# Kernel optimization log

Hardware: AMD Instinct MI355X
Metric: run time of the kernel (lower is better)

The kernel has to match this reference:

```python
import jax, jax.numpy as jnp
import numpy as np

B, T, D, H = 16, 2048, 1024, 1024  # batch, seq (effective block_size), n_embed, head_size


def setup_inputs() -> dict:
    key = jax.random.key(0)
    k1, k2, k3, k4 = jax.random.split(key, 4)
    x = jax.random.normal(k1, (B, T, D), dtype=jnp.float32)
    # torch Linear weight is [out,in]; store as [in,out] for x @ W
    s = 1.0 / np.sqrt(D)
    Wq = jax.random.uniform(k2, (D, H), dtype=jnp.float32, minval=-s, maxval=s)
    Wk = jax.random.uniform(k3, (D, H), dtype=jnp.float32, minval=-s, maxval=s)
    Wv = jax.random.uniform(k4, (D, H), dtype=jnp.float32, minval=-s, maxval=s)
    return {"x": x, "Wq": Wq, "Wk": Wk, "Wv": Wv}


def reference(x, Wq, Wk, Wv):
    # Single-head causal self-attention, NO 1/sqrt(d) scaling (faithful to source).
    q = x @ Wq  # [B,T,H]
    k = x @ Wk  # [B,T,H]
    v = x @ Wv  # [B,T,H]
    w = jnp.einsum('bth,bsh->bts', q, k)  # [B,T,T]
    Tn = x.shape[1]
    causal = jnp.tril(jnp.ones((Tn, Tn), dtype=bool))
    w = jnp.where(causal, w, -jnp.inf)
    w = jax.nn.softmax(w, axis=-1)
    # dropout is identity in eval mode
    out = jnp.einsum('bts,bsh->bth', w, v)  # [B,T,H]
    return out
```

## Files before the change

### kernel.cpp

```cpp
#include <hip/hip_runtime.h>
#include <hip/hip_bf16.h>


typedef _Float16 half8 __attribute__((ext_vector_type(8)));
typedef _Float16 half4v __attribute__((ext_vector_type(4)));
typedef float floatx4 __attribute__((ext_vector_type(4)));

#define TB 16
#define TT 2048
#define TD 1024

#define BARRIER() asm volatile("s_barrier" ::: "memory")

__global__ void cvt_f32_f16(const float* __restrict__ in, _Float16* __restrict__ out, long n) {
    long i = ((long)blockIdx.x * blockDim.x + threadIdx.x) * 4;
    long stride = (long)gridDim.x * blockDim.x * 4;
    for (; i < n; i += stride) {
        float4 f = *(const float4*)(in + i);
        half4v h;
        h[0] = (_Float16)f.x; h[1] = (_Float16)f.y;
        h[2] = (_Float16)f.z; h[3] = (_Float16)f.w;
        *(half4v*)(out + i) = h;
    }
}

__global__ void transpose_cvt_w(const float* __restrict__ in, _Float16* __restrict__ out) {
    __shared__ float tile[32][33];
    const int bx = blockIdx.x * 32, by = blockIdx.y * 32;
    const int tx = threadIdx.x, ty = threadIdx.y;
#pragma unroll
    for (int i = ty; i < 32; i += 8) tile[i][tx] = in[(long)(by + i) * 1024 + bx + tx];
    __syncthreads();
#pragma unroll
    for (int i = ty; i < 32; i += 8) out[(long)(bx + i) * 1024 + by + tx] = (_Float16)tile[tx][i];
}

__device__ __forceinline__ void gload16(const _Float16* g, _Float16* l) {
    __builtin_amdgcn_global_load_lds((const __attribute__((address_space(1))) void*)g,
                                     (__attribute__((address_space(3))) void*)l, 16, 0, 0);
}

template <int MODE>
__global__ __launch_bounds__(512, 2) void gemm256(const _Float16* __restrict__ A,
                                                  const _Float16* __restrict__ B,
                                                  void* __restrict__ Cout,
                                                  void* __restrict__ Cout2,
                                                  int K, int lda, int ldb, int ldc,
                                                  long sAb, long sBb, long sCb,
                                                  int tilesN, int tilesM, int nb) {
    __shared__ _Float16 lds[65536];
    const int tid = threadIdx.x, lane = tid & 63, w = tid >> 6;
    const int wr = w >> 2, wc = w & 3;

    int b, ti, tj;
    if (MODE == 2) {
        const int grp = nb * 4;
        const int g = blockIdx.x / grp;
        ti = tilesM - 1 - g;
        int i2 = blockIdx.x - g * grp;
        const int q = grp >> 3, r = grp & 7, xcd = i2 & 7, idx = i2 >> 3;
        i2 = (xcd < r ? xcd * (q + 1) : r * (q + 1) + (xcd - r) * q) + idx;
        b = i2 >> 2; tj = i2 & 3;
    } else {
        int bx = blockIdx.x;
        const int nwg = gridDim.x, q = nwg >> 3, r = nwg & 7, xcd = bx & 7, idx = bx >> 3;
        bx = (xcd < r ? xcd * (q + 1) : r * (q + 1) + (xcd - r) * q) + idx;
        b = blockIdx.y;
        if (MODE == 1) {
            int rd = bx; ti = 0;
            while (rd > ti) { rd -= ti + 1; ++ti; }
            tj = rd;
        } else {
            ti = bx / tilesN; tj = bx % tilesN;
        }
    }
    A += (long)b * sAb;
    B += (long)b * sBb;
    const long m0 = (long)ti * 256, n0 = (long)tj * 256;
    const int nkt = (MODE == 2) ? (ti + 1) * 4 : (K >> 6);

    const int row0 = tid >> 2;
    const int co   = (((tid & 3) ^ ((tid >> 3) & 3)) << 3);
    const int fcol = ((((lane >> 4) ^ (lane >> 1)) & 3) << 3);
    const int arow = wr * 128 + (lane & 15);
    const int brow = wc * 64 + (lane & 15);

    auto Abase = [&](int buf, int kk) { return lds + ((buf * 2 + kk) << 13); };
    auto Bbase = [&](int buf, int kk) { return lds + 32768 + ((buf * 2 + kk) << 13); };

    auto stageA = [&](int buf, int kk, int kt) {
        const long kb = (long)kt * 64 + kk * 32 + co;
        _Float16* d = Abase(buf, kk) + (w << 9);
        gload16(A + (m0 + row0) * (long)lda + kb, d);
        gload16(A + (m0 + row0 + 128) * (long)lda + kb, d + 4096);
    };
    auto stageB = [&](int buf, int kk, int kt) {
        const long kb = (long)kt * 64 + kk * 32 + co;
        _Float16* d = Bbase(buf, kk) + (w << 9);
        gload16(B + (n0 + row0) * (long)ldb + kb, d);
        gload16(B + (n0 + row0 + 128) * (long)ldb + kb, d + 4096);
    };
    auto ldA = [&](int buf, int kk, int m) {
        return *(const half8*)(Abase(buf, kk) + (arow + m * 16) * 32 + fcol);
    };
    auto ldB = [&](int buf, int kk, int n) {
        return *(const half8*)(Bbase(buf, kk) + (brow + n * 16) * 32 + fcol);
    };

    floatx4 acc[8][4] = {};
    half8 afE[4], afO[4], bfE[4], bfO[4];

#define MFMA_Q(MH, BF, AF)                                                             \
    __builtin_amdgcn_s_setprio(1);                                                     \
    _Pragma("unroll") for (int mm = 0; mm < 4; ++mm)                                   \
    _Pragma("unroll") for (int nn = 0; nn < 4; ++nn)                                   \
        acc[(MH)*4 + mm][nn] =                                                         \
            __builtin_amdgcn_mfma_f32_16x16x32_f16(AF[mm], BF[nn], acc[(MH)*4 + mm][nn], 0, 0, 0); \
    __builtin_amdgcn_s_setprio(0);

    {
        const int k1 = (1 < nkt) ? 1 : nkt - 1;
        stageA(0, 0, 0); stageB(0, 0, 0);
        stageA(0, 1, 0); stageB(0, 1, 0);
        stageA(1, 0, k1); stageB(1, 0, k1);
    }
    asm volatile("s_waitcnt vmcnt(8)" ::: "memory");
    BARRIER();
#pragma unroll
    for (int nn = 0; nn < 4; ++nn) bfE[nn] = ldB(0, 0, nn);
#pragma unroll
    for (int mm = 0; mm < 4; ++mm) afE[mm] = ldA(0, 0, mm);

    for (int t = 0; t < nkt; ++t) {
        const int cur = t & 1, nxt = cur ^ 1;
        const int kt1 = (t + 1 < nkt) ? t + 1 : nkt - 1;
        const int kt2 = (t + 2 < nkt) ? t + 2 : nkt - 1;
        MFMA_Q(0, bfE, afE)
#pragma unroll
        for (int mm = 0; mm < 4; ++mm) afO[mm] = ldA(cur, 0, mm + 4);
        stageA(nxt, 1, kt1);
        asm volatile("s_waitcnt vmcnt(6)" ::: "memory");
        BARRIER();
        MFMA_Q(1, bfE, afO)
#pragma unroll
        for (int nn = 0; nn < 4; ++nn) bfO[nn] = ldB(cur, 1, nn);
#pragma unroll
        for (int mm = 0; mm < 4; ++mm) afE[mm] = ldA(cur, 1, mm);
        stageB(nxt, 1, kt1);
        BARRIER();
        MFMA_Q(0, bfO, afE)
#pragma unroll
        for (int mm = 0; mm < 4; ++mm) afO[mm] = ldA(cur, 1, mm + 4);
        stageA(cur, 0, kt2);
        asm volatile("s_waitcnt vmcnt(6)" ::: "memory");
        BARRIER();
        MFMA_Q(1, bfO, afO)
#pragma unroll
        for (int nn = 0; nn < 4; ++nn) bfE[nn] = ldB(nxt, 0, nn);
#pragma unroll
        for (int mm = 0; mm < 4; ++mm) afE[mm] = ldA(nxt, 0, mm);
        stageB(cur, 0, kt2);
        BARRIER();
    }
#undef MFMA_Q
    asm volatile("s_waitcnt vmcnt(0) lgkmcnt(0)" ::: "memory");

    const int r4 = (lane >> 4) * 4, ccol = lane & 15;
    if (MODE != 2) {
        _Float16* C;
        long nb0 = n0;
        if (MODE == 3 && n0 >= TD) { C = (_Float16*)Cout2; nb0 = n0 - TD; }
        else                        C = (_Float16*)Cout + (long)b * sCb;
#pragma unroll
        for (int m = 0; m < 8; ++m) {
            const long rbase = m0 + wr * 128 + m * 16 + r4;
#pragma unroll
            for (int n = 0; n < 4; ++n) {
                const long cbase = nb0 + wc * 64 + n * 16 + ccol;
#pragma unroll
                for (int j = 0; j < 4; ++j)
                    C[(rbase + j) * (long)ldc + cbase] = (_Float16)acc[m][n][j];
            }
        }
    } else {
        float* C = (float*)Cout + (long)b * sCb;
#pragma unroll
        for (int m = 0; m < 8; ++m) {
            const long rbase = m0 + wr * 128 + m * 16 + r4;
#pragma unroll
            for (int n = 0; n < 4; ++n) {
                const long cbase = n0 + wc * 64 + n * 16 + ccol;
#pragma unroll
                for (int j = 0; j < 4; ++j)
                    C[(rbase + j) * (long)ldc + cbase] = acc[m][n][j];
            }
        }
    }
}

__global__ __launch_bounds__(256) void softmax_rows_f16(_Float16* __restrict__ S, int T) {
    const int wv = threadIdx.x >> 6, lane = threadIdx.x & 63;
    const long row = (long)blockIdx.x * 4 + wv;
    const int t = (int)(row & (T - 1));
    _Float16* s = S + row * (long)T;
    const int nstore = ((t >> 8) + 1) << 8;

    float v[4][8];
    float mx = -__builtin_inff();
#pragma unroll
    for (int c = 0; c < 4; ++c) {
        const int col0 = (c * 64 + lane) * 8;
        if (col0 <= t) {
            half8 hv = *(const half8*)(s + col0);
#pragma unroll
            for (int j = 0; j < 8; ++j) {
                v[c][j] = (col0 + j <= t) ? (float)hv[j] : -__builtin_inff();
                mx = fmaxf(mx, v[c][j]);
            }
        } else {
#pragma unroll
            for (int j = 0; j < 8; ++j) v[c][j] = -__builtin_inff();
        }
    }
#pragma unroll
    for (int o = 32; o; o >>= 1) mx = fmaxf(mx, __shfl_xor(mx, o));

    float sum = 0.f;
#pragma unroll
    for (int c = 0; c < 4; ++c)
#pragma unroll
        for (int j = 0; j < 8; ++j) {
            float p = __expf(v[c][j] - mx);
            v[c][j] = p;
            sum += p;
        }
#pragma unroll
    for (int o = 32; o; o >>= 1) sum += __shfl_xor(sum, o);
    const float inv = 1.f / sum;

#pragma unroll
    for (int c = 0; c < 4; ++c) {
        const int col0 = (c * 64 + lane) * 8;
        if (col0 < nstore) {
            half8 o;
#pragma unroll
            for (int j = 0; j < 8; ++j) o[j] = (_Float16)(v[c][j] * inv);
            *(half8*)(s + col0) = o;
        }
    }
}

extern "C" void kernel_launch(void* const* d_in, const int* in_sizes, int n_in,
                              void* d_out, int out_size, void* d_ws, size_t ws_size,
                              hipStream_t stream) {
    const float* x  = (const float*)d_in[0];
    const float* Wq = (const float*)d_in[1];
    const float* Wk = (const float*)d_in[2];
    const float* Wv = (const float*)d_in[3];
    float* out = (float*)d_out;

    const size_t XB = (size_t)TB * TT * TD;

    _Float16* x16 = (_Float16*)d_out;
    _Float16* Kh  = (_Float16*)d_out + XB;

    char* ws = (char*)d_ws;
    size_t off = 0;
    auto carve = [&](size_t bytes) { char* p = ws + off; off = (off + bytes + 255) & ~(size_t)255; return p; };
    _Float16* wqt = (_Float16*)carve((size_t)TD * TD * 2);
    _Float16* wkt = (_Float16*)carve((size_t)TD * TD * 2);
    _Float16* wvt = (_Float16*)carve((size_t)TD * TD * 2);
    _Float16* Qh  = (_Float16*)carve(XB * 2);
    _Float16* Vt  = (_Float16*)carve(XB * 2);

    const size_t CH = (size_t)TT * TT * 2;
    int NB = 16;
    while (NB > 1 && off + (size_t)NB * CH > ws_size) NB >>= 1;
    _Float16* Sc = (_Float16*)carve((size_t)NB * CH);

    cvt_f32_f16<<<2048, 256, 0, stream>>>(x, x16, (long)XB);
    transpose_cvt_w<<<dim3(32, 32), dim3(32, 8), 0, stream>>>(Wq, wqt);
    transpose_cvt_w<<<dim3(32, 32), dim3(32, 8), 0, stream>>>(Wk, wkt);
    transpose_cvt_w<<<dim3(32, 32), dim3(32, 8), 0, stream>>>(Wv, wvt);

    gemm256<3><<<dim3(128 * 8, 1), 512, 0, stream>>>(x16, wqt, Qh, Kh, TD, TD, TD, TD,
                                                     0, 0, 0, 8, 128, 0);
    gemm256<0><<<dim3(4 * 8, TB), 512, 0, stream>>>(wvt, x16, Vt, nullptr, TD, TD, TD, TT,
                                                    0, (long)TT * TD, (long)TD * TT, 8, 4, 0);

    for (int cb = 0; cb < TB; cb += NB) {
        gemm256<1><<<dim3(36, NB), 512, 0, stream>>>(Qh + (size_t)cb * TT * TD,
                                                     Kh + (size_t)cb * TT * TD, Sc, nullptr,
                                                     TD, TD, TD, TT,
                                                     (long)TT * TD, (long)TT * TD, (long)TT * TT, 8, 8, 0);
        softmax_rows_f16<<<NB * TT / 4, 256, 0, stream>>>(Sc, TT);
        gemm256<2><<<dim3(NB * 32, 1), 512, 0, stream>>>(Sc, Vt + (size_t)cb * TD * TT,
                                                         out + (size_t)cb * TT * TD, nullptr, TT,
                                                         TT, TT, TD,
                                                         (long)TT * TT, (long)TD * TT, (long)TT * TD, 4, 8, NB);
    }
}
```

Before: 473.2 us.

## Switch GEMM inner product to 32x32x16 MFMA tiles with matching fragment layout

Replaces the 16x16x32 f16 MFMA with the 32x32x16 variant. This changes the accumulator shape to 4x2 floatx16 per wave, remaps the LDS fragment loads (row and column swizzle) and rewrites the epilogue's output row mapping. The larger MFMA tile means fewer instructions and fewer LDS operand reads per FLOP. The main loop is also unrolled by 2. The risk is mistakes in the lane-to-element mapping and higher register pressure.

Measured after the change: 497.1 us. 1.05x slower.

```diff
diff --git a/kernel.cpp b/kernel.cpp
--- a/kernel.cpp
+++ b/kernel.cpp
@@ -4,7 +4,7 @@
 
 typedef _Float16 half8 __attribute__((ext_vector_type(8)));
 typedef _Float16 half4v __attribute__((ext_vector_type(4)));
-typedef float floatx4 __attribute__((ext_vector_type(4)));
+typedef float floatx16 __attribute__((ext_vector_type(16)));
 
 #define TB 16
 #define TT 2048
@@ -81,9 +81,9 @@
 
     const int row0 = tid >> 2;
     const int co   = (((tid & 3) ^ ((tid >> 3) & 3)) << 3);
-    const int fcol = ((((lane >> 4) ^ (lane >> 1)) & 3) << 3);
-    const int arow = wr * 128 + (lane & 15);
-    const int brow = wc * 64 + (lane & 15);
+    const int rxor = (lane >> 1) & 3;
+    const int arowb = wr * 128 + (lane & 31);
+    const int browb = wc * 64 + (lane & 31);
 
     auto Abase = [&](int buf, int kk) { return lds + ((buf * 2 + kk) << 13); };
     auto Bbase = [&](int buf, int kk) { return lds + 32768 + ((buf * 2 + kk) << 13); };
@@ -100,22 +100,25 @@
         gload16(B + (n0 + row0) * (long)ldb + kb, d);
         gload16(B + (n0 + row0 + 128) * (long)ldb + kb, d + 4096);
     };
-    auto ldA = [&](int buf, int kk, int m) {
-        return *(const half8*)(Abase(buf, kk) + (arow + m * 16) * 32 + fcol);
+    auto ldA = [&](int buf, int kk, int mt, int kq) {
+        const int fcol = ((((kq << 1) | (lane >> 5)) ^ rxor) << 3);
+        return *(const half8*)(Abase(buf, kk) + (arowb + mt * 32) * 32 + fcol);
     };
-    auto ldB = [&](int buf, int kk, int n) {
-        return *(const half8*)(Bbase(buf, kk) + (brow + n * 16) * 32 + fcol);
+    auto ldB = [&](int buf, int kk, int nt, int kq) {
+        const int fcol = ((((kq << 1) | (lane >> 5)) ^ rxor) << 3);
+        return *(const half8*)(Bbase(buf, kk) + (browb + nt * 32) * 32 + fcol);
     };
 
-    floatx4 acc[8][4] = {};
+    floatx16 acc[4][2] = {};
     half8 afE[4], afO[4], bfE[4], bfO[4];
 
 #define MFMA_Q(MH, BF, AF)                                                             \
     __builtin_amdgcn_s_setprio(1);                                                     \
-    _Pragma("unroll") for (int mm = 0; mm < 4; ++mm)                                   \
-    _Pragma("unroll") for (int nn = 0; nn < 4; ++nn)                                   \
-        acc[(MH)*4 + mm][nn] =                                                         \
-            __builtin_amdgcn_mfma_f32_16x16x32_f16(AF[mm], BF[nn], acc[(MH)*4 + mm][nn], 0, 0, 0); \
+    _Pragma("unroll") for (int kq = 0; kq < 2; ++kq)                                   \
+    _Pragma("unroll") for (int ml = 0; ml < 2; ++ml)                                   \
+    _Pragma("unroll") for (int nt = 0; nt < 2; ++nt)                                   \
+        acc[(MH)*2 + ml][nt] = __builtin_amdgcn_mfma_f32_32x32x16_f16(                 \
+            AF[ml * 2 + kq], BF[nt * 2 + kq], acc[(MH)*2 + ml][nt], 0, 0, 0);          \
     __builtin_amdgcn_s_setprio(0);
 
     {
@@ -127,72 +130,75 @@
     asm volatile("s_waitcnt vmcnt(8)" ::: "memory");
     BARRIER();
 #pragma unroll
-    for (int nn = 0; nn < 4; ++nn) bfE[nn] = ldB(0, 0, nn);
-#pragma unroll
-    for (int mm = 0; mm < 4; ++mm) afE[mm] = ldA(0, 0, mm);
-
+    for (int i = 0; i < 4; ++i) bfE[i] = ldB(0, 0, i >> 1, i & 1);
+#pragma unroll
+    for (int i = 0; i < 4; ++i) afE[i] = ldA(0, 0, i >> 1, i & 1);
+
+#pragma unroll 2
     for (int t = 0; t < nkt; ++t) {
         const int cur = t & 1, nxt = cur ^ 1;
         const int kt1 = (t + 1 < nkt) ? t + 1 : nkt - 1;
         const int kt2 = (t + 2 < nkt) ? t + 2 : nkt - 1;
         MFMA_Q(0, bfE, afE)
 #pragma unroll
-        for (int mm = 0; mm < 4; ++mm) afO[mm] = ldA(cur, 0, mm + 4);
+        for (int i = 0; i < 4; ++i) afO[i] = ldA(cur, 0, 2 + (i >> 1), i & 1);
         stageA(nxt, 1, kt1);
         asm volatile("s_waitcnt vmcnt(6)" ::: "memory");
         BARRIER();
         MFMA_Q(1, bfE, afO)
 #pragma unroll
-        for (int nn = 0; nn < 4; ++nn) bfO[nn] = ldB(cur, 1, nn);
-#pragma unroll
-        for (int mm = 0; mm < 4; ++mm) afE[mm] = ldA(cur, 1, mm);
+        for (int i = 0; i < 4; ++i) bfO[i] = ldB(cur, 1, i >> 1, i & 1);
+#pragma unroll
+        for (int i = 0; i < 4; ++i) afE[i] = ldA(cur, 1, i >> 1, i & 1);
         stageB(nxt, 1, kt1);
         BARRIER();
         MFMA_Q(0, bfO, afE)
 #pragma unroll
-        for (int mm = 0; mm < 4; ++mm) afO[mm] = ldA(cur, 1, mm + 4);
+        for (int i = 0; i < 4; ++i) afO[i] = ldA(cur, 1, 2 + (i >> 1), i & 1);
         stageA(cur, 0, kt2);
         asm volatile("s_waitcnt vmcnt(6)" ::: "memory");
         BARRIER();
         MFMA_Q(1, bfO, afO)
 #pragma unroll
-        for (int nn = 0; nn < 4; ++nn) bfE[nn] = ldB(nxt, 0, nn);
-#pragma unroll
-        for (int mm = 0; mm < 4; ++mm) afE[mm] = ldA(nxt, 0, mm);
+        for (int i = 0; i < 4; ++i) bfE[i] = ldB(nxt, 0, i >> 1, i & 1);
+#pragma unroll
+        for (int i = 0; i < 4; ++i) afE[i] = ldA(nxt, 0, i >> 1, i & 1);
         stageB(cur, 0, kt2);
         BARRIER();
     }
 #undef MFMA_Q
     asm volatile("s_waitcnt vmcnt(0) lgkmcnt(0)" ::: "memory");
 
-    const int r4 = (lane >> 4) * 4, ccol = lane & 15;
+    const int c32 = lane & 31, rh = (lane >> 5) * 4;
     if (MODE != 2) {
         _Float16* C;
         long nb0 = n0;
         if (MODE == 3 && n0 >= TD) { C = (_Float16*)Cout2; nb0 = n0 - TD; }
         else                        C = (_Float16*)Cout + (long)b * sCb;
 #pragma unroll
-        for (int m = 0; m < 8; ++m) {
-            const long rbase = m0 + wr * 128 + m * 16 + r4;
-#pragma unroll
-            for (int n = 0; n < 4; ++n) {
-                const long cbase = nb0 + wc * 64 + n * 16 + ccol;
-#pragma unroll
-                for (int j = 0; j < 4; ++j)
-                    C[(rbase + j) * (long)ldc + cbase] = (_Float16)acc[m][n][j];
+        for (int mt = 0; mt < 4; ++mt) {
+            const long rbase = m0 + wr * 128 + mt * 32 + rh;
+#pragma unroll
+            for (int nt = 0; nt < 2; ++nt) {
+                const long cbase = nb0 + wc * 64 + nt * 32 + c32;
+#pragma unroll
+                for (int r = 0; r < 16; ++r)
+                    C[(rbase + (r & 3) + ((r >> 2) << 3)) * (long)ldc + cbase] =
+                        (_Float16)acc[mt][nt][r];
             }
         }
     } else {
         float* C = (float*)Cout + (long)b * sCb;
 #pragma unroll
-        for (int m = 0; m < 8; ++m) {
-            const long rbase = m0 + wr * 128 + m * 16 + r4;
-#pragma unroll
-            for (int n = 0; n < 4; ++n) {
-                const long cbase = n0 + wc * 64 + n * 16 + ccol;
-#pragma unroll
-                for (int j = 0; j < 4; ++j)
-                    C[(rbase + j) * (long)ldc + cbase] = acc[m][n][j];
+        for (int mt = 0; mt < 4; ++mt) {
+            const long rbase = m0 + wr * 128 + mt * 32 + rh;
+#pragma unroll
+            for (int nt = 0; nt < 2; ++nt) {
+                const long cbase = n0 + wc * 64 + nt * 32 + c32;
+#pragma unroll
+                for (int r = 0; r < 16; ++r)
+                    C[(rbase + (r & 3) + ((r >> 2) << 3)) * (long)ldc + cbase] =
+                        acc[mt][nt][r];
             }
         }
     }
```
